# Kernel optimization log

Measured on AMD Instinct MI355X. Metric: run time of the kernel, lower is better.

The kernel has to match this reference:

```python
import jax, jax.numpy as jnp
import numpy as np

MU = 0            # smeared direction (init arg dir)
IS_ODD = False    # init arg is_odd -> update the EVEN subset
DIMS = (24, 24, 24, 24)
N_PLAQ = 6
PI_2 = 0.6366197723675814  # 2/pi, as in scale_coeff


def setup_inputs() -> dict:
    key = jax.random.key(0)
    k1, k2, k3 = jax.random.split(key, 3)
    shape = (4,) + DIMS + (3, 3)  # [dir, T, Z, Y, X, 3, 3]
    x_re = jax.random.normal(k1, shape, jnp.float32)
    x_im = jax.random.normal(k2, shape, jnp.float32)
    coeff = jax.random.uniform(k3, (N_PLAQ,), jnp.float32)
    return {"x_re": x_re, "x_im": x_im, "coeff": coeff}


def _adj(m):
    return jnp.conj(jnp.swapaxes(m, -1, -2))


def _shift(a, nu, n):
    # lattice .shift(nu, n): value at site + n*nu_hat (periodic); lattice axes are the leading 4
    return jnp.roll(a, -n, axis=nu)


def _eo_filter(dims, is_odd, dtype):
    # evenodd_mask % 2; filter is 1 on the UPDATED subset (odd if is_odd else even)
    grids = jnp.meshgrid(*[jnp.arange(d) for d in dims], indexing='ij')
    parity = sum(grids) % 2
    mask = parity if is_odd else 1 - parity
    return mask.astype(dtype)[..., None, None]


def _matexp(Z, terms=12, squarings=4):
    # scaling-and-squaring Taylor (Horner) matrix exponential, batched over leading dims
    Z = Z * jnp.asarray(0.5 ** squarings, dtype=jnp.float32).astype(Z.dtype)
    eye = jnp.eye(Z.shape[-1], dtype=Z.dtype)
    E = eye
    for k in range(terms, 0, -1):
        E = eye + (Z @ E) / k
    for _ in range(squarings):
        E = E @ E
    return E


def reference(x_re, x_im, coeff):
    x = (x_re + 1j * x_im).astype(jnp.complex64)  # [4, T, Z, Y, X, 3, 3]
    filt = _eo_filter(DIMS, IS_ODD, jnp.complex64)
    # filter_fixed_update: mask mu-links; staples built from fixed-subset x[mu]
    xmu_fix = x[MU] * (1.0 - filt)
    xupd = x[MU] * filt
    # scale_coeff(coeff, 0.75) = (2/pi)*0.75*atan(coeff)
    c = (PI_2 * 0.75) * jnp.arctan(coeff)
    cc = c.astype(jnp.complex64)
    # plaquette staples (n_plaq = 6 loops)
    loops = []
    for nu in range(4):
        if nu == MU:
            continue
        Umu = _shift(xmu_fix, nu, 1)      # x[mu].shift(nu, 1)
        Unu = _shift(x[nu], MU, 1)        # x[nu].shift(mu, 1)
        R = Umu @ _adj(Unu)
        stf = x[nu] @ R                   # forward staple
        L = _adj(x[nu]) @ xmu_fix
        stu = L @ Unu
        loops.append(stf)
        loops.append(_shift(stu, nu, -1)) # backward staple
    f = loops[0] * cc[0]
    for i in range(1, N_PLAQ):
        f = f + loops[i] * cc[i]
    f = f / N_PLAQ
    # stout update on the updated subset: Z = projectTangent(f @ xupd^dag); U' = exp(Z) @ U
    M = f @ _adj(xupd)
    A = 0.5 * (M - _adj(M))               # anti-hermitian part
    tr = jnp.trace(A, axis1=-2, axis2=-1)
    Zt = A - (tr / 3.0)[..., None, None] * jnp.eye(3, dtype=A.dtype)  # traceless
    E = _matexp(Zt)
    ymu = E @ xupd + xmu_fix              # combine updated and fixed subsets
    y = x.at[MU].set(ymu)
    # return real/imag stacked so output is real-valued: [4, T, Z, Y, X, 3, 3, 2]
    return jnp.stack((jnp.real(y), jnp.imag(y)), axis=-1)
```

## Files before the change

### kernel.cpp

```cpp
#include <hip/hip_runtime.h>
#include <cstdint>

#define LT 24
#define NSITE (LT*LT*LT*LT)
#define NCOMPLEX (4*NSITE*9)

struct C3 { float re[9]; float im[9]; };

__device__ __forceinline__ void load9(float* d, const float* __restrict__ p) {
    float4 a, b;
    __builtin_memcpy(&a, p,     16);
    __builtin_memcpy(&b, p + 4, 16);
    d[0]=a.x; d[1]=a.y; d[2]=a.z; d[3]=a.w;
    d[4]=b.x; d[5]=b.y; d[6]=b.z; d[7]=b.w;
    d[8]=p[8];
}

__device__ __forceinline__ void loadM(C3& m, const float* __restrict__ re,
                                      const float* __restrict__ im, int off) {
    load9(m.re, re + off);
    load9(m.im, im + off);
}

__device__ __forceinline__ void storeM(float2* __restrict__ out, int cbase, const C3& m) {
    float4 v;
    v.x=m.re[0]; v.y=m.im[0]; v.z=m.re[1]; v.w=m.im[1];
    __builtin_memcpy(out + cbase,     &v, 16);
    v.x=m.re[2]; v.y=m.im[2]; v.z=m.re[3]; v.w=m.im[3];
    __builtin_memcpy(out + cbase + 2, &v, 16);
    v.x=m.re[4]; v.y=m.im[4]; v.z=m.re[5]; v.w=m.im[5];
    __builtin_memcpy(out + cbase + 4, &v, 16);
    v.x=m.re[6]; v.y=m.im[6]; v.z=m.re[7]; v.w=m.im[7];
    __builtin_memcpy(out + cbase + 6, &v, 16);
    float2 w; w.x=m.re[8]; w.y=m.im[8];
    out[cbase + 8] = w;
}

__device__ __forceinline__ void mmul(C3& o, const C3& a, const C3& b) {
#pragma unroll
    for (int r = 0; r < 3; ++r) {
#pragma unroll
        for (int c = 0; c < 3; ++c) {
            float sr = 0.f, si = 0.f;
#pragma unroll
            for (int k = 0; k < 3; ++k) {
                float ar = a.re[r*3+k], ai = a.im[r*3+k];
                float br = b.re[k*3+c], bi = b.im[k*3+c];
                sr += ar*br - ai*bi;
                si += ar*bi + ai*br;
            }
            o.re[r*3+c] = sr; o.im[r*3+c] = si;
        }
    }
}

__device__ __forceinline__ void mmul_acc(C3& f, const C3& a, const C3& b, float cr) {
#pragma unroll
    for (int r = 0; r < 3; ++r) {
#pragma unroll
        for (int c = 0; c < 3; ++c) {
            float sr = 0.f, si = 0.f;
#pragma unroll
            for (int k = 0; k < 3; ++k) {
                float ar = a.re[r*3+k], ai = a.im[r*3+k];
                float br = b.re[k*3+c], bi = b.im[k*3+c];
                sr += ar*br - ai*bi;
                si += ar*bi + ai*br;
            }
            f.re[r*3+c] += cr * sr; f.im[r*3+c] += cr * si;
        }
    }
}

__device__ __forceinline__ void mmul_adjB(C3& o, const C3& a, const C3& b) {
#pragma unroll
    for (int r = 0; r < 3; ++r) {
#pragma unroll
        for (int c = 0; c < 3; ++c) {
            float sr = 0.f, si = 0.f;
#pragma unroll
            for (int k = 0; k < 3; ++k) {
                float ar = a.re[r*3+k], ai = a.im[r*3+k];
                float br = b.re[c*3+k], bi = b.im[c*3+k];
                sr += ar*br + ai*bi;
                si += ai*br - ar*bi;
            }
            o.re[r*3+c] = sr; o.im[r*3+c] = si;
        }
    }
}

__device__ __forceinline__ void madjA_mul(C3& o, const C3& a, const C3& b) {
#pragma unroll
    for (int r = 0; r < 3; ++r) {
#pragma unroll
        for (int c = 0; c < 3; ++c) {
            float sr = 0.f, si = 0.f;
#pragma unroll
            for (int k = 0; k < 3; ++k) {
                float ar = a.re[k*3+r], ai = a.im[k*3+r];
                float br = b.re[k*3+c], bi = b.im[k*3+c];
                sr += ar*br + ai*bi;
                si += ar*bi - ai*br;
            }
            o.re[r*3+c] = sr; o.im[r*3+c] = si;
        }
    }
}

__device__ __forceinline__ int site_from_idx(int idx, int parity,
                                             int& t, int& z, int& y, int& x) {
    int xh = idx % 12;  int r = idx / 12;
    y = r % LT; r /= LT;
    z = r % LT; t = r / LT;
    x = 2 * xh + ((t + z + y + parity) & 1);
    return ((t * LT + z) * LT + y) * LT + x;
}

__global__ __launch_bounds__(256)
void interleave_copy(const float* __restrict__ xre, const float* __restrict__ xim,
                     float4* __restrict__ out) {
    const float4* __restrict__ re4 = (const float4*)xre;
    const float4* __restrict__ im4 = (const float4*)xim;
    const int nquad  = NCOMPLEX / 4;
    const int stride = gridDim.x * blockDim.x;
    for (int q = blockIdx.x * blockDim.x + threadIdx.x; q < nquad; q += stride) {
        float4 r = re4[q];
        float4 i = im4[q];
        float4 o0, o1;
        o0.x = r.x; o0.y = i.x; o0.z = r.y; o0.w = i.y;
        o1.x = r.z; o1.y = i.z; o1.z = r.w; o1.w = i.w;
        out[2*q]     = o0;
        out[2*q + 1] = o1;
    }
}

__global__ __launch_bounds__(256)
void stout_update(const float* __restrict__ xre, const float* __restrict__ xim,
                  const float* __restrict__ coeff, float2* __restrict__ out) {
    const int idx = blockIdx.x * 256 + threadIdx.x;

    int t, z, y, x;
    const int s = site_from_idx(idx, 0, t, z, y, x);

    float c[6];
#pragma unroll
    for (int i = 0; i < 6; ++i)
        c[i] = 0.07957747154594768f * atanf(coeff[i]);

    int tp = (t + 1 < LT) ? t + 1 : 0;
    int zp = (z + 1 < LT) ? z + 1 : 0;  int zm = (z > 0) ? z - 1 : LT - 1;
    int yp = (y + 1 < LT) ? y + 1 : 0;  int ym = (y > 0) ? y - 1 : LT - 1;
    int xp = (x + 1 < LT) ? x + 1 : 0;  int xm = (x > 0) ? x - 1 : LT - 1;

    const int stt = ((tp * LT + z) * LT + y) * LT + x;
    const int spv[3]  = { ((t  * LT + zp) * LT + y ) * LT + x,
                          ((t  * LT + z ) * LT + yp) * LT + x,
                          ((t  * LT + z ) * LT + y ) * LT + xp };
    const int smv[3]  = { ((t  * LT + zm) * LT + y ) * LT + x,
                          ((t  * LT + z ) * LT + ym) * LT + x,
                          ((t  * LT + z ) * LT + y ) * LT + xm };
    const int smtv[3] = { ((tp * LT + zm) * LT + y ) * LT + x,
                          ((tp * LT + z ) * LT + ym) * LT + x,
                          ((tp * LT + z ) * LT + y ) * LT + xm };

    C3 f;
#pragma unroll
    for (int j = 0; j < 9; ++j) { f.re[j] = 0.f; f.im[j] = 0.f; }

    C3 A, B, Cm, tmp;
#pragma unroll
    for (int i = 0; i < 3; ++i) {
        const int d = i + 1;
        loadM(A, xre, xim, (d * NSITE + s) * 9);
        loadM(B,  xre, xim, (     spv[i])        * 9);
        loadM(Cm, xre, xim, (d * NSITE + stt)    * 9);
        mmul_adjB(tmp, B, Cm);
        mmul_acc(f, A, tmp, c[2 * i]);
        loadM(A,  xre, xim, (d * NSITE + smv[i]) * 9);
        loadM(B,  xre, xim, (     smv[i])        * 9);
        loadM(Cm, xre, xim, (d * NSITE + smtv[i])* 9);
        madjA_mul(tmp, A, B);
        mmul_acc(f, tmp, Cm, c[2 * i + 1]);
    }

    C3 U;
    loadM(U, xre, xim, s * 9);

    C3 Mm;
    mmul_adjB(Mm, f, U);
    C3 Zt;
#pragma unroll
    for (int r = 0; r < 3; ++r) {
#pragma unroll
        for (int cq = 0; cq < 3; ++cq) {
            Zt.re[r*3+cq] = 0.5f * (Mm.re[r*3+cq] - Mm.re[cq*3+r]);
            Zt.im[r*3+cq] = 0.5f * (Mm.im[r*3+cq] + Mm.im[cq*3+r]);
        }
    }
    float trIm = (Zt.im[0] + Zt.im[4] + Zt.im[8]) / 3.0f;
    Zt.im[0] -= trIm; Zt.im[4] -= trIm; Zt.im[8] -= trIm;

#pragma unroll
    for (int j = 0; j < 9; ++j) { Zt.re[j] *= 0.0625f; Zt.im[j] *= 0.0625f; }

    C3 E;
#pragma unroll
    for (int j = 0; j < 9; ++j) { E.re[j] = 0.f; E.im[j] = 0.f; }
    E.re[0] = 1.f; E.re[4] = 1.f; E.re[8] = 1.f;

    C3 Tm;
#pragma unroll
    for (int k = 12; k >= 1; --k) {
        mmul(Tm, Zt, E);
        const float invk = 1.0f / (float)k;
#pragma unroll
        for (int j = 0; j < 9; ++j) {
            E.re[j] = Tm.re[j] * invk;
            E.im[j] = Tm.im[j] * invk;
        }
        E.re[0] += 1.f; E.re[4] += 1.f; E.re[8] += 1.f;
    }
#pragma unroll
    for (int q = 0; q < 4; ++q) {
        mmul(Tm, E, E);
        E = Tm;
    }

    C3 Y;
    mmul(Y, E, U);
    storeM(out, s * 9, Y);
}

extern "C" void kernel_launch(void* const* d_in, const int* in_sizes, int n_in,
                              void* d_out, int out_size, void* d_ws, size_t ws_size,
                              hipStream_t stream) {
    const float* xre   = (const float*)d_in[0];
    const float* xim   = (const float*)d_in[1];
    const float* coeff = (const float*)d_in[2];

    interleave_copy<<<2048, 256, 0, stream>>>(xre, xim, (float4*)d_out);

    const int nblocks = (NSITE / 2) / 256;
    stout_update<<<nblocks, 256, 0, stream>>>(xre, xim, coeff, (float2*)d_out);
}
```

Before: 241.2 us.

## Split stout update into per-direction staple kernel and exponential kernel via workspace

```diff
diff --git a/kernel.cpp b/kernel.cpp
--- a/kernel.cpp
+++ b/kernel.cpp
@@ -3,7 +3,10 @@
 
 #define LT 24
 #define NSITE (LT*LT*LT*LT)
+#define HALF  (NSITE/2)
 #define NCOMPLEX (4*NSITE*9)
+
+typedef float vf4 __attribute__((ext_vector_type(4)));
 
 struct C3 { float re[9]; float im[9]; };
 
@@ -36,6 +39,29 @@
     out[cbase + 8] = w;
 }
 
+__device__ __forceinline__ void store18(float* __restrict__ p, const C3& m) {
+    float4 v;
+    v.x=m.re[0]; v.y=m.re[1]; v.z=m.re[2]; v.w=m.re[3];
+    __builtin_memcpy(p,      &v, 16);
+    v.x=m.re[4]; v.y=m.re[5]; v.z=m.re[6]; v.w=m.re[7];
+    __builtin_memcpy(p + 4,  &v, 16);
+    v.x=m.re[8]; v.y=m.im[0]; v.z=m.im[1]; v.w=m.im[2];
+    __builtin_memcpy(p + 8,  &v, 16);
+    v.x=m.im[3]; v.y=m.im[4]; v.z=m.im[5]; v.w=m.im[6];
+    __builtin_memcpy(p + 12, &v, 16);
+    float2 w; w.x=m.im[7]; w.y=m.im[8];
+    __builtin_memcpy(p + 16, &w, 8);
+}
+
+__device__ __forceinline__ void load18(C3& m, const float* __restrict__ p) {
+    float4 a;
+    __builtin_memcpy(&a, p,      16); m.re[0]=a.x; m.re[1]=a.y; m.re[2]=a.z; m.re[3]=a.w;
+    __builtin_memcpy(&a, p + 4,  16); m.re[4]=a.x; m.re[5]=a.y; m.re[6]=a.z; m.re[7]=a.w;
+    __builtin_memcpy(&a, p + 8,  16); m.re[8]=a.x; m.im[0]=a.y; m.im[1]=a.z; m.im[2]=a.w;
+    __builtin_memcpy(&a, p + 12, 16); m.im[3]=a.x; m.im[4]=a.y; m.im[5]=a.z; m.im[6]=a.w;
+    float2 w; __builtin_memcpy(&w, p + 16, 8); m.im[7]=w.x; m.im[8]=w.y;
+}
+
 __device__ __forceinline__ void mmul(C3& o, const C3& a, const C3& b) {
 #pragma unroll
     for (int r = 0; r < 3; ++r) {
@@ -119,20 +145,141 @@
 
 __global__ __launch_bounds__(256)
 void interleave_copy(const float* __restrict__ xre, const float* __restrict__ xim,
-                     float4* __restrict__ out) {
-    const float4* __restrict__ re4 = (const float4*)xre;
-    const float4* __restrict__ im4 = (const float4*)xim;
+                     vf4* __restrict__ out) {
+    const vf4* __restrict__ re4 = (const vf4*)xre;
+    const vf4* __restrict__ im4 = (const vf4*)xim;
     const int nquad  = NCOMPLEX / 4;
     const int stride = gridDim.x * blockDim.x;
     for (int q = blockIdx.x * blockDim.x + threadIdx.x; q < nquad; q += stride) {
-        float4 r = re4[q];
-        float4 i = im4[q];
-        float4 o0, o1;
-        o0.x = r.x; o0.y = i.x; o0.z = r.y; o0.w = i.y;
-        o1.x = r.z; o1.y = i.z; o1.z = r.w; o1.w = i.w;
-        out[2*q]     = o0;
-        out[2*q + 1] = o1;
-    }
+        vf4 r = re4[q];
+        vf4 i = im4[q];
+        vf4 o0 = { r.x, i.x, r.y, i.y };
+        vf4 o1 = { r.z, i.z, r.w, i.w };
+        __builtin_nontemporal_store(o0, out + 2*q);
+        __builtin_nontemporal_store(o1, out + 2*q + 1);
+    }
+}
+
+__global__ __launch_bounds__(256)
+void stout_staples(const float* __restrict__ xre, const float* __restrict__ xim,
+                   const float* __restrict__ coeff, float* __restrict__ ws) {
+    const int gid = blockIdx.x * 256 + threadIdx.x;
+    const int i   = gid / HALF;
+    const int idx = gid - i * HALF;
+    const int d   = i + 1;
+
+    int t, z, y, x;
+    const int s = site_from_idx(idx, 0, t, z, y, x);
+
+    const float c2  = 0.07957747154594768f * atanf(coeff[2*i]);
+    const float c2p = 0.07957747154594768f * atanf(coeff[2*i + 1]);
+
+    const int tp = (t + 1 < LT) ? t + 1 : 0;
+    const int stt = ((tp * LT + z) * LT + y) * LT + x;
+
+    int sp, sm, smt;
+    if (i == 0) {
+        const int zp = (z + 1 < LT) ? z + 1 : 0;
+        const int zm = (z > 0) ? z - 1 : LT - 1;
+        sp  = ((t  * LT + zp) * LT + y) * LT + x;
+        sm  = ((t  * LT + zm) * LT + y) * LT + x;
+        smt = ((tp * LT + zm) * LT + y) * LT + x;
+    } else if (i == 1) {
+        const int yp = (y + 1 < LT) ? y + 1 : 0;
+        const int ym = (y > 0) ? y - 1 : LT - 1;
+        sp  = ((t  * LT + z) * LT + yp) * LT + x;
+        sm  = ((t  * LT + z) * LT + ym) * LT + x;
+        smt = ((tp * LT + z) * LT + ym) * LT + x;
+    } else {
+        const int xp = (x + 1 < LT) ? x + 1 : 0;
+        const int xm = (x > 0) ? x - 1 : LT - 1;
+        sp  = ((t  * LT + z) * LT + y) * LT + xp;
+        sm  = ((t  * LT + z) * LT + y) * LT + xm;
+        smt = ((tp * LT + z) * LT + y) * LT + xm;
+    }
+
+    C3 A, B, Cm, tmp, pf;
+#pragma unroll
+    for (int j = 0; j < 9; ++j) { pf.re[j] = 0.f; pf.im[j] = 0.f; }
+
+    loadM(B,  xre, xim, sp * 9);
+    loadM(Cm, xre, xim, (d * NSITE + stt) * 9);
+    mmul_adjB(tmp, B, Cm);
+    loadM(A, xre, xim, (d * NSITE + s) * 9);
+    mmul_acc(pf, A, tmp, c2);
+
+    loadM(A, xre, xim, (d * NSITE + sm) * 9);
+    loadM(B, xre, xim, sm * 9);
+    madjA_mul(tmp, A, B);
+    loadM(Cm, xre, xim, (d * NSITE + smt) * 9);
+    mmul_acc(pf, tmp, Cm, c2p);
+
+    store18(ws + (size_t)(i * HALF + idx) * 18, pf);
+}
+
+__global__ __launch_bounds__(256)
+void stout_exp(const float* __restrict__ xre, const float* __restrict__ xim,
+               const float* __restrict__ ws, float2* __restrict__ out) {
+    const int idx = blockIdx.x * 256 + threadIdx.x;
+
+    int t, z, y, x;
+    const int s = site_from_idx(idx, 0, t, z, y, x);
+
+    C3 f, p;
+    load18(f, ws + (size_t)idx * 18);
+    load18(p, ws + (size_t)(HALF + idx) * 18);
+#pragma unroll
+    for (int j = 0; j < 9; ++j) { f.re[j] += p.re[j]; f.im[j] += p.im[j]; }
+    load18(p, ws + (size_t)(2 * HALF + idx) * 18);
+#pragma unroll
+    for (int j = 0; j < 9; ++j) { f.re[j] += p.re[j]; f.im[j] += p.im[j]; }
+
+    C3 U;
+    loadM(U, xre, xim, s * 9);
+
+    C3 Mm;
+    mmul_adjB(Mm, f, U);
+    C3 Zt;
+#pragma unroll
+    for (int r = 0; r < 3; ++r) {
+#pragma unroll
+        for (int cq = 0; cq < 3; ++cq) {
+            Zt.re[r*3+cq] = 0.5f * (Mm.re[r*3+cq] - Mm.re[cq*3+r]);
+            Zt.im[r*3+cq] = 0.5f * (Mm.im[r*3+cq] + Mm.im[cq*3+r]);
+        }
+    }
+    float trIm = (Zt.im[0] + Zt.im[4] + Zt.im[8]) / 3.0f;
+    Zt.im[0] -= trIm; Zt.im[4] -= trIm; Zt.im[8] -= trIm;
+
+#pragma unroll
+    for (int j = 0; j < 9; ++j) { Zt.re[j] *= 0.0625f; Zt.im[j] *= 0.0625f; }
+
+    C3 E;
+#pragma unroll
+    for (int j = 0; j < 9; ++j) { E.re[j] = 0.f; E.im[j] = 0.f; }
+    E.re[0] = 1.f; E.re[4] = 1.f; E.re[8] = 1.f;
+
+    C3 Tm;
+#pragma unroll
+    for (int k = 12; k >= 1; --k) {
+        mmul(Tm, Zt, E);
+        const float invk = 1.0f / (float)k;
+#pragma unroll
+        for (int j = 0; j < 9; ++j) {
+            E.re[j] = Tm.re[j] * invk;
+            E.im[j] = Tm.im[j] * invk;
+        }
+        E.re[0] += 1.f; E.re[4] += 1.f; E.re[8] += 1.f;
+    }
+#pragma unroll
+    for (int q = 0; q < 4; ++q) {
+        mmul(Tm, E, E);
+        E = Tm;
+    }
+
+    C3 Y;
+    mmul(Y, E, U);
+    storeM(out, s * 9, Y);
 }
 
 __global__ __launch_bounds__(256)
@@ -179,8 +326,8 @@
         mmul_acc(f, A, tmp, c[2 * i]);
         loadM(A,  xre, xim, (d * NSITE + smv[i]) * 9);
         loadM(B,  xre, xim, (     smv[i])        * 9);
+        madjA_mul(tmp, A, B);
         loadM(Cm, xre, xim, (d * NSITE + smtv[i])* 9);
-        madjA_mul(tmp, A, B);
         mmul_acc(f, tmp, Cm, c[2 * i + 1]);
     }
 
@@ -239,8 +386,15 @@
     const float* xim   = (const float*)d_in[1];
     const float* coeff = (const float*)d_in[2];
 
-    interleave_copy<<<2048, 256, 0, stream>>>(xre, xim, (float4*)d_out);
-
-    const int nblocks = (NSITE / 2) / 256;
-    stout_update<<<nblocks, 256, 0, stream>>>(xre, xim, coeff, (float2*)d_out);
-}
+    interleave_copy<<<4096, 256, 0, stream>>>(xre, xim, (vf4*)d_out);
+
+    const size_t ws_needed = (size_t)3 * HALF * 18 * sizeof(float);
+    if (ws_size >= ws_needed && d_ws != nullptr) {
+        stout_staples<<<(3 * HALF) / 256, 256, 0, stream>>>(
+            xre, xim, coeff, (float*)d_ws);
+        stout_exp<<<HALF / 256, 256, 0, stream>>>(
+            xre, xim, (const float*)d_ws, (float2*)d_out);
+    } else {
+        stout_update<<<HALF / 256, 256, 0, stream>>>(xre, xim, coeff, (float2*)d_out);
+    }
+}
```

Result: slower. 263.6 us (+9.3%).
